# Performance work log

Measured on AMD Instinct MI355X. Metric: run time of the kernel, lower is better.

Reference implementation:

```python
import jax, jax.numpy as jnp
import numpy as np

# Static config (matches init_kwargs / input_specs)
B, P, A, D, K = 8, 1, 8, 8, 3          # batch, num_plans, action_channels, dim_qk, receptive_field
T, H, W = 32, 32, 32                   # 3D grid
PAD = K // 2
PA = P * A
PAD_VALUE = 0.0


def _pad3(t, val=PAD_VALUE):
    # pad last three (spatial) dims by PAD on each side
    return jnp.pad(t, ((0, 0), (0, 0), (PAD, PAD), (PAD, PAD), (PAD, PAD)), constant_values=val)


def _conv3d(x, w):
    # x: [B, Ci, T, H, W], w: [Co, Ci, K, K, K], VALID padding (input pre-padded)
    return jax.lax.conv_general_dilated(
        x, w, window_strides=(1, 1, 1), padding='VALID',
        dimension_numbers=('NCDHW', 'OIDHW', 'NCDHW'))


def setup_inputs() -> dict:
    key = jax.random.key(0)
    k1, k2, k3, k4 = jax.random.split(key, 4)
    s = 1.0 / np.sqrt(P * K ** 3)  # conv fan-in init scale
    return {
        'values':  jax.random.normal(k1, (B, P, T, H, W), jnp.float32),
        'rewards': jax.random.normal(k2, (B, P, T, H, W), jnp.float32),
        'w_qk':    jax.random.normal(k3, (2 * PA * D, P, K, K, K), jnp.float32) * s,
        'w_v':     jax.random.normal(k4, (PA, P, K, K, K), jnp.float32) * s,
    }


def reference(values, rewards, w_qk, w_v):
    x = values + rewards                       # [B, P, T, H, W]
    xp = _pad3(x)

    qk = _conv3d(xp, w_qk)                     # [B, 2*PA*D, T, H, W]
    q, k = jnp.split(qk, 2, axis=1)            # each [B, PA*D, T, H, W]

    # softmax value-conv weights over the flattened 3D kernel per (out, in) pair
    wv = jax.nn.softmax(w_v.reshape(PA, P, K ** 3), axis=-1).reshape(w_v.shape)
    v = _conv3d(xp, wv)                        # [B, PA, T, H, W]

    kp, vp = _pad3(k), _pad3(v)
    thw = T * H * W
    qf = q.reshape(B, PA, D, thw)              # [B, A, D, thw]

    # local 3x3x3 neighborhood attention: per kernel offset, dot q with shifted k
    # (same math as unfoldNd + einsum, without the K^3*D memory blow-up)
    sims, vns = [], []
    for dt in range(K):
        for dh in range(K):
            for dw in range(K):
                ksh = jax.lax.slice(kp, (0, 0, dt, dh, dw),
                                    (B, PA * D, dt + T, dh + H, dw + W)).reshape(B, PA, D, thw)
                sims.append(jnp.einsum('badt,badt->bat', qf, ksh))
                vns.append(jax.lax.slice(vp, (0, 0, dt, dh, dw),
                                         (B, PA, dt + T, dh + H, dw + W)).reshape(B, PA, thw))

    sim = jnp.stack(sims, axis=-1)             # [B, A, thw, K^3]
    attn = jax.nn.softmax(sim, axis=-1)
    vn = jnp.stack(vns, axis=2)                # [B, A, K^3, thw]
    q_values = jnp.einsum('batn,bant->bat', attn, vn)  # [B, A, thw]

    q_values = q_values.reshape(B, P, A, T, H, W)
    # ActionSelector with soft_maxpool=False: hard max over actions
    next_values = jnp.max(q_values, axis=2)    # [B, P, T, H, W]
    return next_values
```

## Files before the change

kernel.cpp:

```cpp
#include <hip/hip_runtime.h>
#include <hip/hip_bf16.h>

#define NB   8
#define NA   8
#define ND   8
#define NCH  64
#define GT   32
#define KREG 216
#define IMS  40

#define XS_OFF   0
#define BTS_OFF  2048
#define IMC_OFF  13568
#define KP_OFF   0
#define VP_OFF   27648
#define QP_OFF   31104
#define PT_OFF   39424
#define POOL_SZ  40448

typedef _Float16 h2_t  __attribute__((ext_vector_type(2)));
typedef _Float16 f16x8 __attribute__((ext_vector_type(8)));
typedef float    f32x4 __attribute__((ext_vector_type(4)));

static __device__ __forceinline__ unsigned pack_h2(float a, float b) {
#if __has_builtin(__builtin_amdgcn_cvt_pkrtz)
    return __builtin_bit_cast(unsigned, __builtin_amdgcn_cvt_pkrtz(a, b));
#else
    unsigned short ha = __builtin_bit_cast(unsigned short, (_Float16)a);
    unsigned short hb = __builtin_bit_cast(unsigned short, (_Float16)b);
    return (unsigned)ha | ((unsigned)hb << 16);
#endif
}

static __device__ __forceinline__ float dot2(unsigned k, unsigned q, float c) {
#if __has_builtin(__builtin_amdgcn_fdot2)
    return __builtin_amdgcn_fdot2(__builtin_bit_cast(h2_t, k),
                                  __builtin_bit_cast(h2_t, q), c, false);
#else
    h2_t a = __builtin_bit_cast(h2_t, k), b = __builtin_bit_cast(h2_t, q);
    return c + (float)a[0] * (float)b[0] + (float)a[1] * (float)b[1];
#endif
}

__launch_bounds__(256, 4)
__global__ void avi_kernel(const float* __restrict__ values,
                           const float* __restrict__ rewards,
                           const float* __restrict__ w_qk,
                           const float* __restrict__ w_v,
                           float* __restrict__ out) {
    __shared__ __align__(16) char pool[POOL_SZ];
    float*    xS   = (float*)(pool + XS_OFF);
    _Float16* BTSl = (_Float16*)(pool + BTS_OFF);
    _Float16* imc  = (_Float16*)(pool + IMC_OFF);
    unsigned* kPl  = (unsigned*)(pool + KP_OFF);
    _Float16* vPl  = (_Float16*)(pool + VP_OFF);
    unsigned* qPl  = (unsigned*)(pool + QP_OFF);

    const int tid  = threadIdx.x;
    const int bb   = blockIdx.x >> 9;
    const int tile = blockIdx.x & 511;
    const int tz = tile >> 6, ty = (tile >> 3) & 7, tx = tile & 7;
    const int g0z = tz * 4, g0y = ty * 4, g0x = tx * 4;
    const int base_in = bb * (GT * GT * GT);

    for (int i = tid; i < 512; i += 256) {
        int lz = i >> 6, ly = (i >> 3) & 7, lx = i & 7;
        int gz = g0z + lz - 2, gy = g0y + ly - 2, gx = g0x + lx - 2;
        float v = 0.f;
        if ((unsigned)gz < 32u && (unsigned)gy < 32u && (unsigned)gx < 32u) {
            int idx = base_in + gz * 1024 + gy * 32 + gx;
            v = values[idx] + rewards[idx];
        }
        xS[i] = v;
    }
    if (tid < 144) {
        float r[28];
        r[27] = 0.f;
        if (tid < 64) {
            const float* w = w_qk + (NCH + tid) * 27;
            #pragma unroll
            for (int j = 0; j < 27; ++j) r[j] = w[j];
        } else if (tid < 72) {
            int a = tid - 64;
            float m = -1e30f;
            #pragma unroll
            for (int j = 0; j < 27; ++j) { r[j] = w_v[a * 27 + j]; m = fmaxf(m, r[j]); }
            float s = 0.f;
            #pragma unroll
            for (int j = 0; j < 27; ++j) { r[j] = __expf(r[j] - m); s += r[j]; }
            float inv = 1.f / s;
            #pragma unroll
            for (int j = 0; j < 27; ++j) r[j] *= inv;
        } else if (tid < 80) {
            #pragma unroll
            for (int j = 0; j < 27; ++j) r[j] = 0.f;
        } else {
            const float* w = w_qk + (tid - 80) * 27;
            const float L2E = 1.44269504f;
            #pragma unroll
            for (int j = 0; j < 27; ++j) r[j] = w[j] * L2E;
        }
        unsigned* dst = (unsigned*)(BTSl + tid * IMS);
        #pragma unroll
        for (int p = 0; p < 14; ++p) dst[p] = pack_h2(r[2 * p], r[2 * p + 1]);
        #pragma unroll
        for (int p = 14; p < 20; ++p) dst[p] = 0u;
    }
    __syncthreads();

    if (tid < 224) {
        unsigned rowU[16];
        if (tid < KREG) {
            int vz = tid / 36, rem = tid - vz * 36, vy = rem / 6, vx = rem - vy * 6;
            int gz = g0z + vz - 1, gy = g0y + vy - 1, gx = g0x + vx - 1;
            float mask = ((unsigned)gz < 32u && (unsigned)gy < 32u && (unsigned)gx < 32u)
                             ? 1.f : 0.f;
            float xr[27];
            #pragma unroll
            for (int t = 0; t < 27; ++t) {
                int dz = t / 9, dy = (t / 3) % 3, dx = t % 3;
                xr[t] = xS[(vz + dz) * 64 + (vy + dy) * 8 + (vx + dx)] * mask;
            }
            #pragma unroll
            for (int p = 0; p < 13; ++p) rowU[p] = pack_h2(xr[2 * p], xr[2 * p + 1]);
            rowU[13] = pack_h2(xr[26], 0.f);
            rowU[14] = rowU[15] = 0u;
        } else {
            #pragma unroll
            for (int p = 0; p < 16; ++p) rowU[p] = 0u;
        }
        int4* dst = (int4*)((char*)imc + tid * (IMS * 2));
        dst[0] = make_int4(rowU[0], rowU[1], rowU[2], rowU[3]);
        dst[1] = make_int4(rowU[4], rowU[5], rowU[6], rowU[7]);
        dst[2] = make_int4(rowU[8], rowU[9], rowU[10], rowU[11]);
        dst[3] = make_int4(rowU[12], rowU[13], rowU[14], rowU[15]);
    }

    const int lane = tid & 63;
    const int wave = tid >> 6;
    const int quad = lane >> 4;
    const int l15  = lane & 15;

    f16x8 af[9];
    #pragma unroll
    for (int mt = 0; mt < 9; ++mt)
        af[mt] = *(const f16x8*)(BTSl + (mt * 16 + l15) * IMS + quad * 8);

    __syncthreads();

    f16x8 bf[4];
    #pragma unroll
    for (int i = 0; i < 4; ++i) {
        int nt = wave + i * 4;
        if (nt < 14)
            bf[i] = *(const f16x8*)(imc + (nt * 16 + l15) * IMS + quad * 8);
    }

    __syncthreads();

    for (int i = 0; i < 4; ++i) {
        int nt = wave + i * 4;
        if (nt >= 14) break;
        int n = nt * 16 + l15;
        bool nvalid = (n < KREG);
        int vz = n / 36, rm = n - vz * 36, vy = rm / 6, vx = rm - vy * 6;
        bool ctr = ((unsigned)(vz - 1) < 4u) && ((unsigned)(vy - 1) < 4u) &&
                   ((unsigned)(vx - 1) < 4u);
        int cvox = (vz - 1) * 16 + (vy - 1) * 4 + (vx - 1);
        #pragma unroll
        for (int mt = 0; mt < 9; ++mt) {
            f32x4 d = __builtin_amdgcn_mfma_f32_16x16x32_f16(
                af[mt], bf[i], (f32x4){0.f, 0.f, 0.f, 0.f}, 0, 0, 0);
            if (mt < 4) {
                if (nvalid) {
                    int pc0 = mt * 8 + quad * 2;
                    kPl[pc0 * 216 + n]       = pack_h2(d[0], d[1]);
                    kPl[(pc0 + 1) * 216 + n] = pack_h2(d[2], d[3]);
                }
            } else if (mt == 4) {
                if (nvalid && quad < 2) {
                    #pragma unroll
                    for (int j = 0; j < 4; ++j)
                        vPl[(quad * 4 + j) * 216 + n] = (_Float16)d[j];
                }
            } else {
                if (ctr) {
                    int pc0 = (mt - 5) * 8 + quad * 2;
                    qPl[pc0 * 65 + cvox]       = pack_h2(d[0], d[1]);
                    qPl[(pc0 + 1) * 65 + cvox] = pack_h2(d[2], d[3]);
                }
            }
        }
    }
    __syncthreads();

    const int clz = lane >> 4, cly = (lane >> 2) & 3, clx = lane & 3;
    const int rbase = clz * 36 + cly * 6 + clx;

    float best = -1e30f;
    #pragma unroll
    for (int ti = 0; ti < 2; ++ti) {
        int a = wave + ti * 4;
        unsigned qp[4];
        #pragma unroll
        for (int p = 0; p < 4; ++p)
            qp[p] = qPl[(a * 4 + p) * 65 + lane];
        const unsigned* kA = kPl + a * 4 * 216 + rbase;
        const _Float16* vA = vPl + a * 216 + rbase;
        float ssum = 0.f, acc = 0.f;
        #pragma unroll
        for (int nn = 0; nn < 27; ++nn) {
            int dz = nn / 9, dy = (nn / 3) % 3, dx = nn % 3;
            int off = dz * 36 + dy * 6 + dx;
            float s = dot2(kA[off], qp[0],
                      dot2(kA[off + 216], qp[1],
                      dot2(kA[off + 432], qp[2],
                      dot2(kA[off + 648], qp[3], 0.f))));
            float e = exp2f(s);
            float fv = (float)vA[off];
            ssum += e;
            acc = fmaf(e, fv, acc);
        }
        best = fmaxf(best, acc / ssum);
    }
    ((float*)(pool + PT_OFF))[lane * 4 + wave] = best;
    __syncthreads();

    if (tid < 64) {
        float4 p = *(const float4*)((const float*)(pool + PT_OFF) + tid * 4);
        float mx = fmaxf(fmaxf(p.x, p.y), fmaxf(p.z, p.w));
        int lz2 = tid >> 4, ly2 = (tid >> 2) & 3, lx2 = tid & 3;
        int o = base_in + (g0z + lz2) * 1024 + (g0y + ly2) * 32 + (g0x + lx2);
        out[o] = mx;
    }
}

extern "C" void kernel_launch(void* const* d_in, const int* in_sizes, int n_in,
                              void* d_out, int out_size, void* d_ws, size_t ws_size,
                              hipStream_t stream) {
    const float* values  = (const float*)d_in[0];
    const float* rewards = (const float*)d_in[1];
    const float* w_qk    = (const float*)d_in[2];
    const float* w_v     = (const float*)d_in[3];
    avi_kernel<<<NB * 512, 256, 0, stream>>>(values, rewards, w_qk, w_v,
                                             (float*)d_out);
}
```

Baseline: 108.3 us.

## Restructure attention stage with swizzled K layout, vectorized loads, and split neighborhood work

Changes the LDS layout of K to an action-major, voxel-contiguous 16-byte format with an XOR swizzle on the z parity, so the attention stage can fetch K and V with 128-bit loads. Each thread now handles 4 x-adjacent voxels for one action and reuses the loaded K rows across the 3 dx offsets. The 27 neighbors are split between two thread halves that write partial softmax sums to shared memory, and a final reduction combines them and takes the max over actions. The goal is fewer LDS instructions and fewer bank conflicts. The cost is more registers, an unbalanced 4/5 split of the work, and an extra barrier.

```diff
diff --git a/kernel.cpp b/kernel.cpp
--- a/kernel.cpp
+++ b/kernel.cpp
@@ -9,14 +9,11 @@
 #define KREG 216
 #define IMS  40
 
-#define XS_OFF   0
-#define BTS_OFF  2048
-#define IMC_OFF  13568
-#define KP_OFF   0
+#define KACT_OFF 0
 #define VP_OFF   27648
-#define QP_OFF   31104
-#define PT_OFF   39424
-#define POOL_SZ  40448
+#define QP_OFF   32256
+#define SC_OFF   32256
+#define POOL_SZ  40576
 
 typedef _Float16 h2_t  __attribute__((ext_vector_type(2)));
 typedef _Float16 f16x8 __attribute__((ext_vector_type(8)));
@@ -49,11 +46,9 @@
                            const float* __restrict__ w_v,
                            float* __restrict__ out) {
     __shared__ __align__(16) char pool[POOL_SZ];
-    float*    xS   = (float*)(pool + XS_OFF);
-    _Float16* BTSl = (_Float16*)(pool + BTS_OFF);
-    _Float16* imc  = (_Float16*)(pool + IMC_OFF);
-    unsigned* kPl  = (unsigned*)(pool + KP_OFF);
-    _Float16* vPl  = (_Float16*)(pool + VP_OFF);
+    float*    xS   = (float*)(pool + 0);
+    _Float16* BTSl = (_Float16*)(pool + 2048);
+    _Float16* imc  = (_Float16*)(pool + 13568);
     unsigned* qPl  = (unsigned*)(pool + QP_OFF);
 
     const int tid  = threadIdx.x;
@@ -167,21 +162,25 @@
         bool ctr = ((unsigned)(vz - 1) < 4u) && ((unsigned)(vy - 1) < 4u) &&
                    ((unsigned)(vx - 1) < 4u);
         int cvox = (vz - 1) * 16 + (vy - 1) * 4 + (vx - 1);
+        int kp_byte = (n * 16) ^ ((vz & 1) << 4);
         #pragma unroll
         for (int mt = 0; mt < 9; ++mt) {
             f32x4 d = __builtin_amdgcn_mfma_f32_16x16x32_f16(
                 af[mt], bf[i], (f32x4){0.f, 0.f, 0.f, 0.f}, 0, 0, 0);
             if (mt < 4) {
                 if (nvalid) {
-                    int pc0 = mt * 8 + quad * 2;
-                    kPl[pc0 * 216 + n]       = pack_h2(d[0], d[1]);
-                    kPl[(pc0 + 1) * 216 + n] = pack_h2(d[2], d[3]);
+                    int a = mt * 2 + (quad >> 1);
+                    int2 w2;
+                    w2.x = (int)pack_h2(d[0], d[1]);
+                    w2.y = (int)pack_h2(d[2], d[3]);
+                    *(int2*)(pool + KACT_OFF + a * 3456 + kp_byte + (quad & 1) * 8) = w2;
                 }
             } else if (mt == 4) {
                 if (nvalid && quad < 2) {
                     #pragma unroll
                     for (int j = 0; j < 4; ++j)
-                        vPl[(quad * 4 + j) * 216 + n] = (_Float16)d[j];
+                        *(_Float16*)(pool + VP_OFF + (quad * 4 + j) * 576 +
+                                     vz * 96 + vy * 16 + vx * 2) = (_Float16)d[j];
                 }
             } else {
                 if (ctr) {
@@ -194,44 +193,78 @@
     }
     __syncthreads();
 
-    const int clz = lane >> 4, cly = (lane >> 2) & 3, clx = lane & 3;
-    const int rbase = clz * 36 + cly * 6 + clx;
-
-    float best = -1e30f;
-    #pragma unroll
-    for (int ti = 0; ti < 2; ++ti) {
-        int a = wave + ti * 4;
-        unsigned qp[4];
+    const int a    = (tid >> 4) & 7;
+    const int row  = tid & 15;
+    const int h    = tid >> 7;
+    const int clz2 = row >> 2, cly2 = row & 3;
+
+    unsigned qp[4][4];
+    #pragma unroll
+    for (int x = 0; x < 4; ++x) {
         #pragma unroll
         for (int p = 0; p < 4; ++p)
-            qp[p] = qPl[(a * 4 + p) * 65 + lane];
-        const unsigned* kA = kPl + a * 4 * 216 + rbase;
-        const _Float16* vA = vPl + a * 216 + rbase;
-        float ssum = 0.f, acc = 0.f;
-        #pragma unroll
-        for (int nn = 0; nn < 27; ++nn) {
-            int dz = nn / 9, dy = (nn / 3) % 3, dx = nn % 3;
-            int off = dz * 36 + dy * 6 + dx;
-            float s = dot2(kA[off], qp[0],
-                      dot2(kA[off + 216], qp[1],
-                      dot2(kA[off + 432], qp[2],
-                      dot2(kA[off + 648], qp[3], 0.f))));
-            float e = exp2f(s);
-            float fv = (float)vA[off];
-            ssum += e;
-            acc = fmaf(e, fv, acc);
-        }
-        best = fmaxf(best, acc / ssum);
-    }
-    ((float*)(pool + PT_OFF))[lane * 4 + wave] = best;
+            qp[x][p] = qPl[(a * 4 + p) * 65 + row * 4 + x];
+    }
+    __syncthreads();
+
+    float ssum[4] = {0.f, 0.f, 0.f, 0.f};
+    float acc[4]  = {0.f, 0.f, 0.f, 0.f};
+    const char* kbase = pool + KACT_OFF + a * 3456;
+    const char* vbase = pool + VP_OFF  + a * 576;
+
+#define STEP(DZ, DY) do {                                                     \
+        const int zz = clz2 + (DZ), cc = cly2 + (DY);                         \
+        const int zbit = zz & 1;                                              \
+        const char* adrA = kbase + zz * 576 + cc * 96 + zbit * 16;            \
+        const char* adrB = kbase + zz * 576 + cc * 96 + 16 - zbit * 16;       \
+        int4 km[6];                                                           \
+        km[0] = *(const int4*)(adrA);                                         \
+        km[1] = *(const int4*)(adrB);                                         \
+        km[2] = *(const int4*)(adrA + 32);                                    \
+        km[3] = *(const int4*)(adrB + 32);                                    \
+        km[4] = *(const int4*)(adrA + 64);                                    \
+        km[5] = *(const int4*)(adrB + 64);                                    \
+        f16x8 vv = *(const f16x8*)(vbase + zz * 96 + cc * 16);                \
+        _Pragma("unroll")                                                     \
+        for (int x = 0; x < 4; ++x) {                                         \
+            _Pragma("unroll")                                                 \
+            for (int dx = 0; dx < 3; ++dx) {                                  \
+                const int j = x + dx;                                         \
+                float s = dot2((unsigned)km[j].x, qp[x][0],                   \
+                          dot2((unsigned)km[j].y, qp[x][1],                   \
+                          dot2((unsigned)km[j].z, qp[x][2],                   \
+                          dot2((unsigned)km[j].w, qp[x][3], 0.f))));          \
+                float e = exp2f(s);                                           \
+                ssum[x] += e;                                                 \
+                acc[x] = fmaf(e, (float)vv[j], acc[x]);                       \
+            }                                                                 \
+        }                                                                     \
+    } while (0)
+
+    if (h == 0) {
+        STEP(0, 0); STEP(0, 1); STEP(0, 2); STEP(1, 0);
+    } else {
+        STEP(1, 1); STEP(1, 2); STEP(2, 0); STEP(2, 1); STEP(2, 2);
+    }
+#undef STEP
+
+    float2* sc = (float2*)(pool + SC_OFF);
+    #pragma unroll
+    for (int x = 0; x < 4; ++x)
+        sc[(a * 2 + h) * 64 + row * 4 + x] = make_float2(ssum[x], acc[x]);
     __syncthreads();
 
     if (tid < 64) {
-        float4 p = *(const float4*)((const float*)(pool + PT_OFF) + tid * 4);
-        float mx = fmaxf(fmaxf(p.x, p.y), fmaxf(p.z, p.w));
+        float best = -1e30f;
+        #pragma unroll
+        for (int aa = 0; aa < 8; ++aa) {
+            float2 p0 = sc[(aa * 2 + 0) * 64 + tid];
+            float2 p1 = sc[(aa * 2 + 1) * 64 + tid];
+            best = fmaxf(best, (p0.y + p1.y) / (p0.x + p1.x));
+        }
         int lz2 = tid >> 4, ly2 = (tid >> 2) & 3, lx2 = tid & 3;
         int o = base_in + (g0z + lz2) * 1024 + (g0y + ly2) * 32 + (g0x + lx2);
-        out[o] = mx;
+        out[o] = best;
     }
 }
 
```

Result: faster. 104.2 us (-3.8%).
